# Kernel tuning notes

Hardware: AMD Instinct MI355X
Metric: run time of the kernel (lower is better)

## Reference

```python
import jax, jax.numpy as jnp
import numpy as np

B, SEQ, VOCAB = 128, 200, 1400
D = 256          # input_size == hidden_size
H = 256
NCLS = 128


def _p(key, shape, scale=0.05):
    return jax.random.normal(key, shape, dtype=jnp.float32) * scale


def setup_inputs() -> dict:
    key = jax.random.key(0)
    ks = jax.random.split(key, 24)
    inp = {
        "inputs": jax.random.uniform(ks[0], (B, SEQ, VOCAB), dtype=jnp.float32),
        "timestamps": jax.random.uniform(ks[1], (B, SEQ), dtype=jnp.float32),
        "emb": _p(ks[2], (VOCAB, D)),
        # TimeLSTM 1
        "Wall1_w": _p(ks[3], (4 * H, D)), "Wall1_b": _p(ks[4], (4 * H,)),
        "Uall1_w": _p(ks[5], (4 * H, H)), "Uall1_b": _p(ks[6], (4 * H,)),
        "Wd1_w": _p(ks[7], (H, H)), "Wd1_b": _p(ks[8], (H,)),
        # TimeLSTM 2
        "Wall2_w": _p(ks[9], (4 * H, D)), "Wall2_b": _p(ks[10], (4 * H,)),
        "Uall2_w": _p(ks[11], (4 * H, H)), "Uall2_b": _p(ks[12], (4 * H,)),
        "Wd2_w": _p(ks[13], (H, H)), "Wd2_b": _p(ks[14], (H,)),
        # attention / output heads
        "wa_w": _p(ks[15], (1, H)),
        "Wb_w": _p(ks[16], (H, H)),
        "Wout_w": _p(ks[17], (NCLS, H)),
        # initial states (torch.randn in original forward)
        "h01": jax.random.normal(ks[18], (B, H), dtype=jnp.float32),
        "c01": jax.random.normal(ks[19], (B, H), dtype=jnp.float32),
        "h02": jax.random.normal(ks[20], (B, H), dtype=jnp.float32),
        "c02": jax.random.normal(ks[21], (B, H), dtype=jnp.float32),
    }
    return inp


def _time_lstm(embedded, timestamps, h0, c0, Wall_w, Wall_b, Uall_w, Uall_b, Wd_w, Wd_b):
    # Precompute the input projection for all steps (one big GEMM).
    # NOTE: original code applies W_all to h and U_all to x.
    ux = jnp.einsum('bsd,ed->sbe', embedded, Uall_w) + Uall_b  # [seq, b, 4h]
    ts = jnp.swapaxes(timestamps, 0, 1)[:, :, None]            # [seq, b, 1]

    def step(carry, xs):
        h, c = carry
        ux_s, t_s = xs
        c_s1 = jnp.tanh(c @ Wd_w.T + Wd_b)
        c_adj = c - c_s1 + c_s1 * t_s
        gates = jax.nn.sigmoid(h @ Wall_w.T + Wall_b + ux_s)   # all 4 gates sigmoid (incl. c_tmp)
        f, i, o, c_tmp = jnp.split(gates, 4, axis=1)
        c_new = f * c_adj + i * c_tmp
        h_new = o * jnp.tanh(c_new)
        return (h_new, c_new), h_new

    _, hs = jax.lax.scan(step, (h0, c0), (ux, ts))
    return jnp.swapaxes(hs, 0, 1)  # [b, seq, h]


def reference(inputs, timestamps, emb,
              Wall1_w, Wall1_b, Uall1_w, Uall1_b, Wd1_w, Wd1_b,
              Wall2_w, Wall2_b, Uall2_w, Uall2_b, Wd2_w, Wd2_b,
              wa_w, Wb_w, Wout_w, h01, c01, h02, c02):
    embedded = jnp.einsum('bsv,vd->bsd', inputs, emb)  # [b, seq, d]
    out1 = _time_lstm(embedded, timestamps, h01, c01,
                      Wall1_w, Wall1_b, Uall1_w, Uall1_b, Wd1_w, Wd1_b)
    E = jnp.einsum('bsh,h->bs', out1, wa_w[0])
    alpha = jax.nn.softmax(E, axis=1)                  # [b, seq]
    out2 = _time_lstm(embedded, timestamps, h02, c02,
                      Wall2_w, Wall2_b, Uall2_w, Uall2_b, Wd2_w, Wd2_b)
    Beta = jnp.tanh(jnp.einsum('bsh,kh->bsk', out2, Wb_w))  # [b, seq, h]
    ctx = jnp.sum(embedded * Beta * alpha[:, :, None], axis=1)  # [b, h]
    return ctx @ Wout_w.T  # [b, num_classes]
```

## Files before the change

### kernel.cpp

```cpp
#include <hip/hip_runtime.h>

typedef unsigned short u16;
typedef unsigned long long u64;
typedef __attribute__((ext_vector_type(8))) short bf16x8;
typedef __attribute__((ext_vector_type(4))) float f32x4;
typedef __attribute__((ext_vector_type(4))) unsigned short us4;

#define MFMA(a,b,c) __builtin_amdgcn_mfma_f32_16x16x32_bf16((a),(b),(c),0,0,0)
#define KEEP(x) asm volatile("" : "+v"(x))


static __device__ __forceinline__ u16 f2b(float f){
  unsigned u = __float_as_uint(f);
  u += 0x7fffu + ((u >> 16) & 1u);
  return (u16)(u >> 16);
}
static __device__ __forceinline__ float b2f(u16 v){
  return __uint_as_float(((unsigned)v) << 16);
}
static __device__ __forceinline__ float sigm(float x){ return 1.0f/(1.0f+__expf(-x)); }
static __device__ __forceinline__ float tanhx(float x){
  x = fminf(fmaxf(x, -15.f), 15.f);
  float e = __expf(-2.f*x);
  return (1.f - e)/(1.f + e);
}
static __device__ __forceinline__ void gl16(const void* g, void* l){
  __builtin_amdgcn_global_load_lds((const __attribute__((address_space(1))) void*)g,
                                   (__attribute__((address_space(3))) void*)l, 16, 0, 0);
}

__global__ __launch_bounds__(256) void k_prep(
  const float* __restrict__ in0, u16* __restrict__ A0,
  const float* __restrict__ emb, u16* __restrict__ embT,
  const float* __restrict__ s0, const float* __restrict__ s1, const float* __restrict__ s2,
  const float* __restrict__ s3, const float* __restrict__ s4, const float* __restrict__ s5,
  const float* __restrict__ s6,
  u16* __restrict__ d0, u16* __restrict__ d1, u16* __restrict__ d2, u16* __restrict__ d3,
  u16* __restrict__ d4, u16* __restrict__ d5, u16* __restrict__ d6)
{
  int bx = blockIdx.x, tid = threadIdx.x;
  if (bx < 35200){
    long long i4 = (long long)bx*256 + tid;
    long long o = i4*4;
    int r = (int)(o / 1408);
    int c = (int)(o % 1408);
    us4 d;
    if (c + 4 <= 1400){
      f32x4 v = *(const f32x4*)&in0[(long long)r*1400 + c];
      d[0]=f2b(v[0]); d[1]=f2b(v[1]); d[2]=f2b(v[2]); d[3]=f2b(v[3]);
    } else {
      for (int k=0;k<4;k++){ int cc=c+k; d[k] = (cc<1400)? f2b(in0[(long long)r*1400+cc]) : (u16)0; }
    }
    *(us4*)&A0[(long long)r*1408 + c] = d;
  } else if (bx < 36608){
    int idx = (bx-35200)*256 + tid;
    int n = idx / 1408, k = idx % 1408;
    embT[idx] = (k < 1400) ? f2b(emb[(long long)k*256 + n]) : (u16)0;
  } else {
    long long q = (long long)(bx-36608)*256 + tid;
    const float* src; u16* dst; long long rel;
    if      (q < 65536)  { src=s0; dst=d0; rel=q; }
    else if (q < 131072) { src=s1; dst=d1; rel=q-65536; }
    else if (q < 196608) { src=s2; dst=d2; rel=q-131072; }
    else if (q < 262144) { src=s3; dst=d3; rel=q-196608; }
    else if (q < 278528) { src=s4; dst=d4; rel=q-262144; }
    else if (q < 294912) { src=s5; dst=d5; rel=q-278528; }
    else                 { src=s6; dst=d6; rel=q-294912; }
    long long o = rel*4;
    f32x4 v = *(const f32x4*)&src[o];
    us4 d; d[0]=f2b(v[0]); d[1]=f2b(v[1]); d[2]=f2b(v[2]); d[3]=f2b(v[3]);
    *(us4*)&dst[o] = d;
  }
}

__global__ __launch_bounds__(256) void k_init(float* __restrict__ E, float* __restrict__ ctx){
  int i = blockIdx.x*256 + threadIdx.x;
  if (i < 32768) E[i] = 0.f;
  else ctx[i-32768] = 0.f;
}

template<int EPI>
__global__ __launch_bounds__(256) void k_gemm(const u16* __restrict__ A, const u16* __restrict__ Bt,
    int N, int K,
    float* __restrict__ Cf, u16* __restrict__ Cb,
    const float* __restrict__ bias1, const float* __restrict__ bias2,
    const u16* __restrict__ Bt2, u16* __restrict__ Cb2,
    const float* __restrict__ bias3, const float* __restrict__ bias4,
    const float* __restrict__ emb, const float* __restrict__ alpha)
{
  __shared__ __align__(16) u16 As[128*64];
  __shared__ __align__(16) u16 Bs[128*64];
  __shared__ float red[2][128];
  const int tid = threadIdx.x;
  const int l = tid & 63, w = tid >> 6;
  const int quad = l >> 4, lb = l & 15;
  const int wr = w >> 1, wc = w & 1;
  const long long m0 = (long long)blockIdx.x * 128;
  int n0 = blockIdx.y * 128;
  if (EPI==6 && blockIdx.y >= 8){
    Bt = Bt2; Cb = Cb2; bias1 = bias3; bias2 = bias4; n0 = (blockIdx.y-8)*128;
  }

  f32x4 acc[4][4];
  #pragma unroll
  for (int i=0;i<4;i++)
    #pragma unroll
    for (int j=0;j<4;j++) acc[i][j] = (f32x4){0.f,0.f,0.f,0.f};

  for (int kk = 0; kk < K; kk += 64){
    #pragma unroll
    for (int it=0; it<4; ++it){
      int slot = it*256 + tid;
      int m = slot >> 3;
      int q = (slot & 7) ^ (m & 7);
      gl16(A + (m0+m)*K + kk + q*8, &As[slot*8]);
    }
    #pragma unroll
    for (int it=0; it<4; ++it){
      int slot = it*256 + tid;
      int m = slot >> 3;
      int q = (slot & 7) ^ (m & 7);
      gl16(Bt + (long long)(n0+m)*K + kk + q*8, &Bs[slot*8]);
    }
    __syncthreads();
    #pragma unroll
    for (int ks=0; ks<2; ++ks){
      int kq = quad + ks*4;
      bf16x8 af[4], bfr[4];
      #pragma unroll
      for (int i=0;i<4;i++){ int m = wr*64 + i*16 + lb; af[i]  = *(const bf16x8*)&As[m*64 + ((kq ^ (m&7))*8)]; }
      #pragma unroll
      for (int j=0;j<4;j++){ int n = wc*64 + j*16 + lb; bfr[j] = *(const bf16x8*)&Bs[n*64 + ((kq ^ (n&7))*8)]; }
      #pragma unroll
      for (int i=0;i<4;i++)
        #pragma unroll
        for (int j=0;j<4;j++)
          acc[i][j] = MFMA(af[i], bfr[j], acc[i][j]);
    }
    __syncthreads();
  }

  if (EPI==5){
    const int b0 = (int)(m0 / 200);
    red[tid>>7][tid&127] = 0.f;
    __syncthreads();
    #pragma unroll
    for (int i=0;i<4;i++){
      #pragma unroll
      for (int j=0;j<4;j++){
        int col = wc*64 + j*16 + lb;
        #pragma unroll
        for (int r=0;r<4;r++){
          long long row = m0 + wr*64 + i*16 + quad*4 + r;
          long long o = row*N + n0 + col;
          float v = emb[o] * tanhx(acc[i][j][r]) * alpha[row];
          atomicAdd(&red[(int)(row/200) - b0][col], v);
        }
      }
    }
    __syncthreads();
    int bl = tid >> 7, col = tid & 127;
    int bb = b0 + bl;
    if (bb < 128) atomicAdd(&Cf[bb*256 + n0 + col], red[bl][col]);
    return;
  }

  #pragma unroll
  for (int i=0;i<4;i++){
    #pragma unroll
    for (int j=0;j<4;j++){
      int col = n0 + wc*64 + j*16 + lb;
      #pragma unroll
      for (int r=0;r<4;r++){
        long long row = m0 + wr*64 + i*16 + quad*4 + r;
        long long o = row*N + col;
        float v = acc[i][j][r];
        if (EPI==1){ Cf[o]=v; Cb[o]=f2b(v); }
        else if (EPI==6){ Cb[o] = f2b(v + bias1[col] + bias2[col]); }
      }
    }
  }
}

__global__ __launch_bounds__(256,1) void k_scan(
  const u16* __restrict__ Wall1, const u16* __restrict__ Wd1, const float* __restrict__ Wd1b,
  const u16* __restrict__ ux1, const float* __restrict__ h01, const float* __restrict__ c01,
  const u16* __restrict__ Wall2, const u16* __restrict__ Wd2, const float* __restrict__ Wd2b,
  const u16* __restrict__ ux2, const float* __restrict__ h02, const float* __restrict__ c02,
  const float* __restrict__ ts, const float* __restrict__ wa,
  float* __restrict__ E, u16* __restrict__ out2,
  u64* __restrict__ pay)
{
  __shared__ __align__(16) u16 hb[16][264];
  __shared__ __align__(16) u16 cb[16][264];
  const int bi = blockIdx.x;
  const int lstm = bi >> 5;
  const int bc   = (bi >> 2) & 7;
  const int jw   = bi & 3;
  const int grp  = bi >> 2;
  const u16* Wall  = lstm ? Wall2 : Wall1;
  const u16* Wd    = lstm ? Wd2   : Wd1;
  const float* Wdb = lstm ? Wd2b  : Wd1b;
  const u16* ux    = lstm ? ux2   : ux1;
  const float* h0  = lstm ? h02   : h01;
  const float* c0  = lstm ? c02   : c01;

  const int tid = threadIdx.x;
  const int l = tid & 63, w = tid >> 6;
  const int quad = l >> 4, lb = l & 15;
  const int bg = bc*16 + lb;
  const int jwave = jw*64 + w*16;
  const int jlane = jwave + quad*4;
  const int bb = tid >> 4, jj = tid & 15;
  const bool sibR = (jj >> 2) != jw;

  bf16x8 wfA[4][8], wdA[8];
  #pragma unroll
  for (int g=0; g<4; ++g)
    #pragma unroll
    for (int kk=0; kk<8; ++kk){
      wfA[g][kk] = *(const bf16x8*)&Wall[(long long)(g*256 + jwave + lb)*256 + kk*32 + quad*8];
      KEEP(wfA[g][kk]);
    }
  #pragma unroll
  for (int kk=0; kk<8; ++kk){
    wdA[kk] = *(const bf16x8*)&Wd[(long long)(jwave + lb)*256 + kk*32 + quad*8];
    KEEP(wdA[kk]);
  }

  f32x4 bcs  = *(const f32x4*)&Wdb[jlane];
  f32x4 wav  = *(const f32x4*)&wa[jlane];
  f32x4 creg = *(const f32x4*)&c0[(long long)bg*256 + jlane];

  {
    int j0 = jj*16;
    #pragma unroll
    for (int kq=0; kq<4; ++kq){
      f32x4 hv = *(const f32x4*)&h0[(long long)(bc*16+bb)*256 + j0 + kq*4];
      f32x4 cv = *(const f32x4*)&c0[(long long)(bc*16+bb)*256 + j0 + kq*4];
      us4 hp0, cp0;
      #pragma unroll
      for (int r=0;r<4;++r){ hp0[r]=f2b(hv[r]); cp0[r]=f2b(cv[r]); }
      *(us4*)&hb[bb][j0+kq*4] = hp0;
      *(us4*)&cb[bb][j0+kq*4] = cp0;
    }
  }
  __syncthreads();

  us4 uxr[4];
  #pragma unroll
  for (int g=0; g<4; ++g)
    uxr[g] = *(const us4*)&ux[(long long)bg*200*1024 + g*256 + jlane];
  float tcur = ts[(long long)bg*200];

  for (int s=0; s<200; ++s){
    f32x4 ag[4];
    #pragma unroll
    for (int g=0; g<4; ++g)
      #pragma unroll
      for (int r=0; r<4; ++r) ag[g][r] = b2f(uxr[g][r]);
    float tnx = 0.f;
    if (s < 199){
      #pragma unroll
      for (int g=0; g<4; ++g)
        uxr[g] = *(const us4*)&ux[((long long)bg*200 + s+1)*1024 + g*256 + jlane];
      tnx = ts[(long long)bg*200 + s+1];
    }
    f32x4 ad = bcs;
    #pragma unroll
    for (int kk=0;kk<8;++kk){
      bf16x8 cf = *(const bf16x8*)&cb[lb][kk*32 + quad*8];
      ad = MFMA(wdA[kk], cf, ad);
    }
    #pragma unroll
    for (int kk=0;kk<8;++kk){
      bf16x8 hf = *(const bf16x8*)&hb[lb][kk*32 + quad*8];
      #pragma unroll
      for (int g=0; g<4; ++g) ag[g] = MFMA(wfA[g][kk], hf, ag[g]);
    }
    f32x4 hn; us4 hp, cp;
    #pragma unroll
    for (int r=0;r<4;++r){
      float cs1 = tanhx(ad[r]);
      float cadj = creg[r] + cs1*(tcur - 1.0f);
      float fg = sigm(ag[0][r]);
      float ig = sigm(ag[1][r]);
      float og = sigm(ag[2][r]);
      float cg = sigm(ag[3][r]);
      float cn = fg*cadj + ig*cg;
      float hv = og*tanhx(cn);
      creg[r]=cn; hn[r]=hv;
      hp[r]=f2b(hv); cp[r]=f2b(cn);
    }
    tcur = tnx;
    if (s < 199){
      const u64 tag = (u64)(s+1);
      const int slot = (s+1)&1;
      long long pw = ((((long long)(slot*16+grp))*16 + lb)*64 + (jlane>>2))*3;
      u64 w0 = (u64)hp[0] | ((u64)hp[1]<<16) | ((u64)hp[2]<<32) | (tag<<48);
      u64 w1 = (u64)hp[3] | ((u64)cp[0]<<16) | ((u64)cp[1]<<32) | (tag<<48);
      u64 w2 = (u64)cp[2] | ((u64)cp[3]<<16) | (tag<<48);
      __hip_atomic_store(&pay[pw],   w0, __ATOMIC_RELAXED, __HIP_MEMORY_SCOPE_AGENT);
      __hip_atomic_store(&pay[pw+1], w1, __ATOMIC_RELAXED, __HIP_MEMORY_SCOPE_AGENT);
      __hip_atomic_store(&pay[pw+2], w2, __ATOMIC_RELAXED, __HIP_MEMORY_SCOPE_AGENT);
    }
    if (lstm==0){
      float e = hn[0]*wav[0] + hn[1]*wav[1] + hn[2]*wav[2] + hn[3]*wav[3];
      e += __shfl_xor(e, 16, 64);
      e += __shfl_xor(e, 32, 64);
      if (l < 16) atomicAdd(&E[(long long)bg*256 + s], e);
    } else {
      *(us4*)&out2[((long long)bg*200 + s)*256 + jlane] = hp;
    }
    if (s < 199){
      const u64 tag = (u64)(s+1);
      const int slot = (s+1)&1;
      asm volatile("s_barrier" ::: "memory");
      *(us4*)&hb[lb][jlane] = hp;
      *(us4*)&cb[lb][jlane] = cp;
      if (sibR){
        long long rb = (((long long)(slot*16+grp))*16 + bb)*192 + (long long)jj*12;
        u64 W[12];
        for (;;){
          #pragma unroll
          for (int i=0;i<12;++i)
            W[i] = __hip_atomic_load(&pay[rb+i], __ATOMIC_RELAXED, __HIP_MEMORY_SCOPE_AGENT);
          bool ok = true;
          #pragma unroll
          for (int i=0;i<12;++i) ok &= ((W[i]>>48) == tag);
          if (ok) break;
          __builtin_amdgcn_s_sleep(1);
        }
        #pragma unroll
        for (int i=0;i<4;++i){
          u64 w0=W[i*3], w1=W[i*3+1], w2=W[i*3+2];
          us4 hv, cv;
          hv[0]=(u16)w0; hv[1]=(u16)(w0>>16); hv[2]=(u16)(w0>>32); hv[3]=(u16)w1;
          cv[0]=(u16)(w1>>16); cv[1]=(u16)(w1>>32); cv[2]=(u16)w2; cv[3]=(u16)(w2>>16);
          *(us4*)&hb[bb][jj*16+i*4] = hv;
          *(us4*)&cb[bb][jj*16+i*4] = cv;
        }
      }
      asm volatile("s_waitcnt lgkmcnt(0)\n\ts_barrier" ::: "memory");
    }
  }
}

__global__ __launch_bounds__(256) void k_attn(const float* __restrict__ E, float* __restrict__ alpha){
  __shared__ float buf[256];
  int b = blockIdx.x, tid = threadIdx.x;
  float Ev = (tid < 200) ? E[(long long)b*256 + tid] : -1e30f;
  buf[tid]=Ev; __syncthreads();
  for (int st=128; st>0; st>>=1){ if (tid<st) buf[tid]=fmaxf(buf[tid],buf[tid+st]); __syncthreads(); }
  float mx = buf[0]; __syncthreads();
  float e = (tid<200)? __expf(Ev-mx) : 0.f;
  buf[tid]=e; __syncthreads();
  for (int st=128; st>0; st>>=1){ if (tid<st) buf[tid]+=buf[tid+st]; __syncthreads(); }
  float sm = buf[0];
  if (tid<200) alpha[(long long)b*200+tid] = e/sm;
}

__global__ __launch_bounds__(128) void k_out(const float* __restrict__ ctx, const float* __restrict__ Wout,
                                             float* __restrict__ out){
  __shared__ float cs[256];
  int b = blockIdx.x, t = threadIdx.x;
  cs[t] = ctx[b*256+t]; cs[t+128] = ctx[b*256+t+128];
  __syncthreads();
  const float* wr = Wout + (long long)t*256;
  float a0=0,a1=0,a2=0,a3=0;
  for (int j=0;j<256;j+=4){
    f32x4 v = *(const f32x4*)&wr[j];
    a0+=v[0]*cs[j]; a1+=v[1]*cs[j+1]; a2+=v[2]*cs[j+2]; a3+=v[3]*cs[j+3];
  }
  out[(long long)b*128 + t] = (a0+a1)+(a2+a3);
}

extern "C" void kernel_launch(void* const* d_in, const int* in_sizes, int n_in,
                              void* d_out, int out_size, void* d_ws, size_t ws_size,
                              hipStream_t stream)
{
  (void)in_sizes; (void)n_in; (void)out_size; (void)ws_size;
  const float* inputs = (const float*)d_in[0];
  const float* tstamp = (const float*)d_in[1];
  const float* emb    = (const float*)d_in[2];
  const float* Wall1w = (const float*)d_in[3];
  const float* Wall1b = (const float*)d_in[4];
  const float* Uall1w = (const float*)d_in[5];
  const float* Uall1b = (const float*)d_in[6];
  const float* Wd1w   = (const float*)d_in[7];
  const float* Wd1b   = (const float*)d_in[8];
  const float* Wall2w = (const float*)d_in[9];
  const float* Wall2b = (const float*)d_in[10];
  const float* Uall2w = (const float*)d_in[11];
  const float* Uall2b = (const float*)d_in[12];
  const float* Wd2w   = (const float*)d_in[13];
  const float* Wd2b   = (const float*)d_in[14];
  const float* wa     = (const float*)d_in[15];
  const float* Wbw    = (const float*)d_in[16];
  const float* Woutw  = (const float*)d_in[17];
  const float* h01    = (const float*)d_in[18];
  const float* c01    = (const float*)d_in[19];
  const float* h02    = (const float*)d_in[20];
  const float* c02    = (const float*)d_in[21];

  char* ws = (char*)d_ws;
  u16*   ux1   = (u16*)  (ws + 0);
  u16*   ux2   = (u16*)  (ws + 52428800LL);
  float* embF  = (float*)(ws + 104857600LL);
  u16*   embB  = (u16*)  (ws + 131072000LL);
  char*  scr   =          ws + 144179200LL;
  u16*   A0    = (u16*)scr;
  u16*   out2  = (u16*)  (scr + 0);
  float* E     = (float*)(scr + 13107200LL);
  float* ctx   = (float*)(scr + 13238272LL);
  float* alpha = (float*)(scr + 13369344LL);
  u64*   pay   = (u64*)  (scr + 13471744LL);
  u16* embT    = (u16*)(ws + 216268800LL);
  u16* Wall1B  = (u16*)(ws + 216989696LL);
  u16* Wall2B  = (u16*)(ws + 217513984LL);
  u16* Uall1B  = (u16*)(ws + 218038272LL);
  u16* Uall2B  = (u16*)(ws + 218562560LL);
  u16* Wd1B    = (u16*)(ws + 219086848LL);
  u16* Wd2B    = (u16*)(ws + 219217920LL);
  u16* WbB     = (u16*)(ws + 219348992LL);

  k_prep<<<37824, 256, 0, stream>>>(inputs, A0, emb, embT,
                                    Wall1w, Wall2w, Uall1w, Uall2w, Wd1w, Wd2w, Wbw,
                                    Wall1B, Wall2B, Uall1B, Uall2B, Wd1B, Wd2B, WbB);
  k_gemm<1><<<dim3(200,2), 256, 0, stream>>>(A0, embT, 256, 1408, embF, embB,
                                             nullptr, nullptr, nullptr, nullptr,
                                             nullptr, nullptr, nullptr, nullptr);
  k_gemm<6><<<dim3(200,16), 256, 0, stream>>>(embB, Uall1B, 1024, 256, nullptr, ux1,
                                              Uall1b, Wall1b,
                                              Uall2B, ux2, Uall2b, Wall2b,
                                              nullptr, nullptr);
  k_init<<<256, 256, 0, stream>>>(E, ctx);
  k_scan<<<64, 256, 0, stream>>>(Wall1B, Wd1B, Wd1b, ux1, h01, c01,
                                 Wall2B, Wd2B, Wd2b, ux2, h02, c02,
                                 tstamp, wa, E, out2, pay);
  k_attn<<<128, 256, 0, stream>>>(E, alpha);
  k_gemm<5><<<dim3(200,2), 256, 0, stream>>>(out2, WbB, 256, 256, ctx, nullptr,
                                             nullptr, nullptr, nullptr, nullptr,
                                             nullptr, nullptr, embF, alpha);
  k_out<<<128, 128, 0, stream>>>(ctx, Woutw, (float*)d_out);
}
```

Before: 1.289 ms.

## Process two batch chunks per scan block and halve the scan grid

Each scan block now handles two 16-row batch chunks with the same register-resident weights, using separate LDS buffers and cell-state registers for each chunk. The grid drops from 64 to 32 blocks, so fewer blocks take part in the per-step cross-block handshake, and the MFMA work of one chunk can overlap the memory latency of the other. In exchange each block does twice the serial work per step and polls two payload slots, which lengthens the critical path of the recurrence.

```diff
diff --git a/kernel.cpp b/kernel.cpp
--- a/kernel.cpp
+++ b/kernel.cpp
@@ -191,13 +191,17 @@
   float* __restrict__ E, u16* __restrict__ out2,
   u64* __restrict__ pay)
 {
-  __shared__ __align__(16) u16 hb[16][264];
-  __shared__ __align__(16) u16 cb[16][264];
+  __shared__ __align__(16) u16 hbA[16][264];
+  __shared__ __align__(16) u16 cbA[16][264];
+  __shared__ __align__(16) u16 hbB[16][264];
+  __shared__ __align__(16) u16 cbB[16][264];
   const int bi = blockIdx.x;
-  const int lstm = bi >> 5;
-  const int bc   = (bi >> 2) & 7;
+  const int lstm = bi >> 4;
+  const int bp   = (bi >> 2) & 3;
   const int jw   = bi & 3;
-  const int grp  = bi >> 2;
+  const int cA = bp*2, cB = bp*2+1;
+  const int grpA = lstm*8 + cA;
+  const int grpB = lstm*8 + cB;
   const u16* Wall  = lstm ? Wall2 : Wall1;
   const u16* Wd    = lstm ? Wd2   : Wd1;
   const float* Wdb = lstm ? Wd2b  : Wd1b;
@@ -208,7 +212,8 @@
   const int tid = threadIdx.x;
   const int l = tid & 63, w = tid >> 6;
   const int quad = l >> 4, lb = l & 15;
-  const int bg = bc*16 + lb;
+  const int bgA = cA*16 + lb;
+  const int bgB = cB*16 + lb;
   const int jwave = jw*64 + w*16;
   const int jlane = jwave + quad*4;
   const int bb = tid >> 4, jj = tid & 15;
@@ -230,101 +235,169 @@
 
   f32x4 bcs  = *(const f32x4*)&Wdb[jlane];
   f32x4 wav  = *(const f32x4*)&wa[jlane];
-  f32x4 creg = *(const f32x4*)&c0[(long long)bg*256 + jlane];
+  f32x4 cregA = *(const f32x4*)&c0[(long long)bgA*256 + jlane];
+  f32x4 cregB = *(const f32x4*)&c0[(long long)bgB*256 + jlane];
 
   {
     int j0 = jj*16;
     #pragma unroll
     for (int kq=0; kq<4; ++kq){
-      f32x4 hv = *(const f32x4*)&h0[(long long)(bc*16+bb)*256 + j0 + kq*4];
-      f32x4 cv = *(const f32x4*)&c0[(long long)(bc*16+bb)*256 + j0 + kq*4];
+      f32x4 hv = *(const f32x4*)&h0[(long long)(cA*16+bb)*256 + j0 + kq*4];
+      f32x4 cv = *(const f32x4*)&c0[(long long)(cA*16+bb)*256 + j0 + kq*4];
       us4 hp0, cp0;
       #pragma unroll
       for (int r=0;r<4;++r){ hp0[r]=f2b(hv[r]); cp0[r]=f2b(cv[r]); }
-      *(us4*)&hb[bb][j0+kq*4] = hp0;
-      *(us4*)&cb[bb][j0+kq*4] = cp0;
+      *(us4*)&hbA[bb][j0+kq*4] = hp0;
+      *(us4*)&cbA[bb][j0+kq*4] = cp0;
+      hv = *(const f32x4*)&h0[(long long)(cB*16+bb)*256 + j0 + kq*4];
+      cv = *(const f32x4*)&c0[(long long)(cB*16+bb)*256 + j0 + kq*4];
+      #pragma unroll
+      for (int r=0;r<4;++r){ hp0[r]=f2b(hv[r]); cp0[r]=f2b(cv[r]); }
+      *(us4*)&hbB[bb][j0+kq*4] = hp0;
+      *(us4*)&cbB[bb][j0+kq*4] = cp0;
     }
   }
   __syncthreads();
 
-  us4 uxr[4];
+  us4 uxrA[4], uxrB[4];
   #pragma unroll
-  for (int g=0; g<4; ++g)
-    uxr[g] = *(const us4*)&ux[(long long)bg*200*1024 + g*256 + jlane];
-  float tcur = ts[(long long)bg*200];
+  for (int g=0; g<4; ++g){
+    uxrA[g] = *(const us4*)&ux[(long long)bgA*200*1024 + g*256 + jlane];
+    uxrB[g] = *(const us4*)&ux[(long long)bgB*200*1024 + g*256 + jlane];
+  }
+  float tcurA = ts[(long long)bgA*200];
+  float tcurB = ts[(long long)bgB*200];
 
   for (int s=0; s<200; ++s){
-    f32x4 ag[4];
-    #pragma unroll
-    for (int g=0; g<4; ++g)
-      #pragma unroll
-      for (int r=0; r<4; ++r) ag[g][r] = b2f(uxr[g][r]);
-    float tnx = 0.f;
+    const u64 tag = (u64)(s+1);
+    const int slot = (s+1)&1;
+    us4 hpA, cpA, hpB, cpB;
+    {
+      f32x4 ag[4];
+      #pragma unroll
+      for (int g=0; g<4; ++g)
+        #pragma unroll
+        for (int r=0; r<4; ++r) ag[g][r] = b2f(uxrA[g][r]);
+      if (s < 199){
+        #pragma unroll
+        for (int g=0; g<4; ++g)
+          uxrA[g] = *(const us4*)&ux[((long long)bgA*200 + s+1)*1024 + g*256 + jlane];
+      }
+      f32x4 ad = bcs;
+      #pragma unroll
+      for (int kk=0;kk<8;++kk){
+        bf16x8 cf = *(const bf16x8*)&cbA[lb][kk*32 + quad*8];
+        ad = MFMA(wdA[kk], cf, ad);
+      }
+      #pragma unroll
+      for (int kk=0;kk<8;++kk){
+        bf16x8 hf = *(const bf16x8*)&hbA[lb][kk*32 + quad*8];
+        #pragma unroll
+        for (int g=0; g<4; ++g) ag[g] = MFMA(wfA[g][kk], hf, ag[g]);
+      }
+      f32x4 hn;
+      #pragma unroll
+      for (int r=0;r<4;++r){
+        float cs1 = tanhx(ad[r]);
+        float cadj = cregA[r] + cs1*(tcurA - 1.0f);
+        float fg = sigm(ag[0][r]);
+        float ig = sigm(ag[1][r]);
+        float og = sigm(ag[2][r]);
+        float cg = sigm(ag[3][r]);
+        float cn = fg*cadj + ig*cg;
+        float hv = og*tanhx(cn);
+        cregA[r]=cn; hn[r]=hv;
+        hpA[r]=f2b(hv); cpA[r]=f2b(cn);
+      }
+      if (s < 199){
+        tcurA = ts[(long long)bgA*200 + s+1];
+        long long pw = ((((long long)(slot*16+grpA))*16 + lb)*64 + (jlane>>2))*3;
+        u64 w0 = (u64)hpA[0] | ((u64)hpA[1]<<16) | ((u64)hpA[2]<<32) | (tag<<48);
+        u64 w1 = (u64)hpA[3] | ((u64)cpA[0]<<16) | ((u64)cpA[1]<<32) | (tag<<48);
+        u64 w2 = (u64)cpA[2] | ((u64)cpA[3]<<16) | (tag<<48);
+        __hip_atomic_store(&pay[pw],   w0, __ATOMIC_RELAXED, __HIP_MEMORY_SCOPE_AGENT);
+        __hip_atomic_store(&pay[pw+1], w1, __ATOMIC_RELAXED, __HIP_MEMORY_SCOPE_AGENT);
+        __hip_atomic_store(&pay[pw+2], w2, __ATOMIC_RELAXED, __HIP_MEMORY_SCOPE_AGENT);
+      }
+      if (lstm==0){
+        float e = hn[0]*wav[0] + hn[1]*wav[1] + hn[2]*wav[2] + hn[3]*wav[3];
+        e += __shfl_xor(e, 16, 64);
+        e += __shfl_xor(e, 32, 64);
+        if (l < 16) atomicAdd(&E[(long long)bgA*256 + s], e);
+      } else {
+        *(us4*)&out2[((long long)bgA*200 + s)*256 + jlane] = hpA;
+      }
+    }
+    {
+      f32x4 ag[4];
+      #pragma unroll
+      for (int g=0; g<4; ++g)
+        #pragma unroll
+        for (int r=0; r<4; ++r) ag[g][r] = b2f(uxrB[g][r]);
+      if (s < 199){
+        #pragma unroll
+        for (int g=0; g<4; ++g)
+          uxrB[g] = *(const us4*)&ux[((long long)bgB*200 + s+1)*1024 + g*256 + jlane];
+      }
+      f32x4 ad = bcs;
+      #pragma unroll
+      for (int kk=0;kk<8;++kk){
+        bf16x8 cf = *(const bf16x8*)&cbB[lb][kk*32 + quad*8];
+        ad = MFMA(wdA[kk], cf, ad);
+      }
+      #pragma unroll
+      for (int kk=0;kk<8;++kk){
+        bf16x8 hf = *(const bf16x8*)&hbB[lb][kk*32 + quad*8];
+        #pragma unroll
+        for (int g=0; g<4; ++g) ag[g] = MFMA(wfA[g][kk], hf, ag[g]);
+      }
+      f32x4 hn;
+      #pragma unroll
+      for (int r=0;r<4;++r){
+        float cs1 = tanhx(ad[r]);
+        float cadj = cregB[r] + cs1*(tcurB - 1.0f);
+        float fg = sigm(ag[0][r]);
+        float ig = sigm(ag[1][r]);
+        float og = sigm(ag[2][r]);
+        float cg = sigm(ag[3][r]);
+        float cn = fg*cadj + ig*cg;
+        float hv = og*tanhx(cn);
+        cregB[r]=cn; hn[r]=hv;
+        hpB[r]=f2b(hv); cpB[r]=f2b(cn);
+      }
+      if (s < 199){
+        tcurB = ts[(long long)bgB*200 + s+1];
+        long long pw = ((((long long)(slot*16+grpB))*16 + lb)*64 + (jlane>>2))*3;
+        u64 w0 = (u64)hpB[0] | ((u64)hpB[1]<<16) | ((u64)hpB[2]<<32) | (tag<<48);
+        u64 w1 = (u64)hpB[3] | ((u64)cpB[0]<<16) | ((u64)cpB[1]<<32) | (tag<<48);
+        u64 w2 = (u64)cpB[2] | ((u64)cpB[3]<<16) | (tag<<48);
+        __hip_atomic_store(&pay[pw],   w0, __ATOMIC_RELAXED, __HIP_MEMORY_SCOPE_AGENT);
+        __hip_atomic_store(&pay[pw+1], w1, __ATOMIC_RELAXED, __HIP_MEMORY_SCOPE_AGENT);
+        __hip_atomic_store(&pay[pw+2], w2, __ATOMIC_RELAXED, __HIP_MEMORY_SCOPE_AGENT);
+      }
+      if (lstm==0){
+        float e = hn[0]*wav[0] + hn[1]*wav[1] + hn[2]*wav[2] + hn[3]*wav[3];
+        e += __shfl_xor(e, 16, 64);
+        e += __shfl_xor(e, 32, 64);
+        if (l < 16) atomicAdd(&E[(long long)bgB*256 + s], e);
+      } else {
+        *(us4*)&out2[((long long)bgB*200 + s)*256 + jlane] = hpB;
+      }
+    }
     if (s < 199){
-      #pragma unroll
-      for (int g=0; g<4; ++g)
-        uxr[g] = *(const us4*)&ux[((long long)bg*200 + s+1)*1024 + g*256 + jlane];
-      tnx = ts[(long long)bg*200 + s+1];
-    }
-    f32x4 ad = bcs;
-    #pragma unroll
-    for (int kk=0;kk<8;++kk){
-      bf16x8 cf = *(const bf16x8*)&cb[lb][kk*32 + quad*8];
-      ad = MFMA(wdA[kk], cf, ad);
-    }
-    #pragma unroll
-    for (int kk=0;kk<8;++kk){
-      bf16x8 hf = *(const bf16x8*)&hb[lb][kk*32 + quad*8];
-      #pragma unroll
-      for (int g=0; g<4; ++g) ag[g] = MFMA(wfA[g][kk], hf, ag[g]);
-    }
-    f32x4 hn; us4 hp, cp;
-    #pragma unroll
-    for (int r=0;r<4;++r){
-      float cs1 = tanhx(ad[r]);
-      float cadj = creg[r] + cs1*(tcur - 1.0f);
-      float fg = sigm(ag[0][r]);
-      float ig = sigm(ag[1][r]);
-      float og = sigm(ag[2][r]);
-      float cg = sigm(ag[3][r]);
-      float cn = fg*cadj + ig*cg;
-      float hv = og*tanhx(cn);
-      creg[r]=cn; hn[r]=hv;
-      hp[r]=f2b(hv); cp[r]=f2b(cn);
-    }
-    tcur = tnx;
-    if (s < 199){
-      const u64 tag = (u64)(s+1);
-      const int slot = (s+1)&1;
-      long long pw = ((((long long)(slot*16+grp))*16 + lb)*64 + (jlane>>2))*3;
-      u64 w0 = (u64)hp[0] | ((u64)hp[1]<<16) | ((u64)hp[2]<<32) | (tag<<48);
-      u64 w1 = (u64)hp[3] | ((u64)cp[0]<<16) | ((u64)cp[1]<<32) | (tag<<48);
-      u64 w2 = (u64)cp[2] | ((u64)cp[3]<<16) | (tag<<48);
-      __hip_atomic_store(&pay[pw],   w0, __ATOMIC_RELAXED, __HIP_MEMORY_SCOPE_AGENT);
-      __hip_atomic_store(&pay[pw+1], w1, __ATOMIC_RELAXED, __HIP_MEMORY_SCOPE_AGENT);
-      __hip_atomic_store(&pay[pw+2], w2, __ATOMIC_RELAXED, __HIP_MEMORY_SCOPE_AGENT);
-    }
-    if (lstm==0){
-      float e = hn[0]*wav[0] + hn[1]*wav[1] + hn[2]*wav[2] + hn[3]*wav[3];
-      e += __shfl_xor(e, 16, 64);
-      e += __shfl_xor(e, 32, 64);
-      if (l < 16) atomicAdd(&E[(long long)bg*256 + s], e);
-    } else {
-      *(us4*)&out2[((long long)bg*200 + s)*256 + jlane] = hp;
-    }
-    if (s < 199){
-      const u64 tag = (u64)(s+1);
-      const int slot = (s+1)&1;
       asm volatile("s_barrier" ::: "memory");
-      *(us4*)&hb[lb][jlane] = hp;
-      *(us4*)&cb[lb][jlane] = cp;
+      *(us4*)&hbA[lb][jlane] = hpA;
+      *(us4*)&cbA[lb][jlane] = cpA;
+      *(us4*)&hbB[lb][jlane] = hpB;
+      *(us4*)&cbB[lb][jlane] = cpB;
       if (sibR){
-        long long rb = (((long long)(slot*16+grp))*16 + bb)*192 + (long long)jj*12;
+        long long rbA = (((long long)(slot*16+grpA))*16 + bb)*192 + (long long)jj*12;
+        long long rbB = (((long long)(slot*16+grpB))*16 + bb)*192 + (long long)jj*12;
         u64 W[12];
         for (;;){
           #pragma unroll
           for (int i=0;i<12;++i)
-            W[i] = __hip_atomic_load(&pay[rb+i], __ATOMIC_RELAXED, __HIP_MEMORY_SCOPE_AGENT);
+            W[i] = __hip_atomic_load(&pay[rbA+i], __ATOMIC_RELAXED, __HIP_MEMORY_SCOPE_AGENT);
           bool ok = true;
           #pragma unroll
           for (int i=0;i<12;++i) ok &= ((W[i]>>48) == tag);
@@ -337,8 +410,27 @@
           us4 hv, cv;
           hv[0]=(u16)w0; hv[1]=(u16)(w0>>16); hv[2]=(u16)(w0>>32); hv[3]=(u16)w1;
           cv[0]=(u16)(w1>>16); cv[1]=(u16)(w1>>32); cv[2]=(u16)w2; cv[3]=(u16)(w2>>16);
-          *(us4*)&hb[bb][jj*16+i*4] = hv;
-          *(us4*)&cb[bb][jj*16+i*4] = cv;
+          *(us4*)&hbA[bb][jj*16+i*4] = hv;
+          *(us4*)&cbA[bb][jj*16+i*4] = cv;
+        }
+        for (;;){
+          #pragma unroll
+          for (int i=0;i<12;++i)
+            W[i] = __hip_atomic_load(&pay[rbB+i], __ATOMIC_RELAXED, __HIP_MEMORY_SCOPE_AGENT);
+          bool ok = true;
+          #pragma unroll
+          for (int i=0;i<12;++i) ok &= ((W[i]>>48) == tag);
+          if (ok) break;
+          __builtin_amdgcn_s_sleep(1);
+        }
+        #pragma unroll
+        for (int i=0;i<4;++i){
+          u64 w0=W[i*3], w1=W[i*3+1], w2=W[i*3+2];
+          us4 hv, cv;
+          hv[0]=(u16)w0; hv[1]=(u16)(w0>>16); hv[2]=(u16)(w0>>32); hv[3]=(u16)w1;
+          cv[0]=(u16)(w1>>16); cv[1]=(u16)(w1>>32); cv[2]=(u16)w2; cv[3]=(u16)(w2>>16);
+          *(us4*)&hbB[bb][jj*16+i*4] = hv;
+          *(us4*)&cbB[bb][jj*16+i*4] = cv;
         }
       }
       asm volatile("s_waitcnt lgkmcnt(0)\n\ts_barrier" ::: "memory");
@@ -435,7 +527,7 @@
                                               Uall2B, ux2, Uall2b, Wall2b,
                                               nullptr, nullptr);
   k_init<<<256, 256, 0, stream>>>(E, ctx);
-  k_scan<<<64, 256, 0, stream>>>(Wall1B, Wd1B, Wd1b, ux1, h01, c01,
+  k_scan<<<32, 256, 0, stream>>>(Wall1B, Wd1B, Wd1b, ux1, h01, c01,
                                  Wall2B, Wd2B, Wd2b, ux2, h02, c02,
                                  tstamp, wa, E, out2, pay);
   k_attn<<<128, 256, 0, stream>>>(E, alpha);
```

Result: slower. 1.849 ms (+43.5%).
